# Optimization experiments

Measured on AMD Instinct MI355X. Metric: run time of the kernel, lower is better.

## Reference

```python
import jax, jax.numpy as jnp
import numpy as np


def setup_inputs() -> dict:
    key = jax.random.key(0)
    ks = jax.random.split(key, 8)
    B, T, D, H = 4, 4096, 1024, 64
    scale = D ** -0.5
    return {
        "x": jax.random.normal(ks[0], (B, T, D), dtype=jnp.float32),
        "mask": jax.random.randint(ks[1], (B, T), 0, 2, dtype=jnp.int32),
        "wq": jax.random.normal(ks[2], (H, D), dtype=jnp.float32) * scale,
        "bq": jax.random.normal(ks[3], (H,), dtype=jnp.float32) * 0.02,
        "wk": jax.random.normal(ks[4], (H, D), dtype=jnp.float32) * scale,
        "bk": jax.random.normal(ks[5], (H,), dtype=jnp.float32) * 0.02,
        "wv": jax.random.normal(ks[6], (H, D), dtype=jnp.float32) * scale,
        "bv": jax.random.normal(ks[7], (H,), dtype=jnp.float32) * 0.02,
    }


def reference(x, mask, wq, bq, wk, bk, wv, bv):
    # x: [B,T,D]; wq/wk/wv: [H,D] (torch Linear convention), mask: [B,T] int
    head_size = wq.shape[0]
    q = jnp.einsum("btd,hd->bth", x, wq) + bq  # [B,T,H]
    k = jnp.einsum("btd,hd->bth", x, wk) + bk
    v = jnp.einsum("btd,hd->bth", x, wv) + bv
    attn = jnp.einsum("bth,bsh->bts", q, k) * (head_size ** -0.5)  # [B,T,T]
    pad_mask = mask.astype(bool)[:, None, :]  # [B,1,T], True = keep
    attn = jnp.where(pad_mask, attn, jnp.float32(-1e9))
    attn = jax.nn.softmax(attn, axis=-1)
    # dropout is identity in eval/deterministic mode
    return jnp.einsum("bts,bsh->bth", attn, v)  # [B,T,H]
```

## Files before the change

kernel.cpp:

```cpp
#include <hip/hip_runtime.h>
#include <math.h>

#define BATCH 4
#define SEQ   4096
#define DIM   1024
#define HEAD  64
#define MROWS (BATCH*SEQ)
#define KT    64
#define QBLK  64

typedef __attribute__((ext_vector_type(8))) short short8;
typedef __attribute__((ext_vector_type(4))) float f32x4;

static __device__ __forceinline__ unsigned short f2b(float f) {
    union { float f; unsigned u; } v; v.f = f;
    return (unsigned short)((v.u + 0x7FFFu + ((v.u >> 16) & 1u)) >> 16);
}
static __device__ __forceinline__ unsigned cvtpk(float a, float b) {
    unsigned r;
    asm("v_cvt_pk_bf16_f32 %0, %1, %2" : "=v"(r) : "v"(a), "v"(b));
    return r;
}

#define QSC (0.125f * 1.4426950408889634f)
__global__ __launch_bounds__(256) void wconv_kernel(
    const float* __restrict__ wq, const float* __restrict__ bq,
    const float* __restrict__ wk, const float* __restrict__ bk,
    const float* __restrict__ wv, const float* __restrict__ bv,
    unsigned short* __restrict__ Wb, float* __restrict__ biasAll)
{
    int idx = blockIdx.x * 256 + threadIdx.x;
    int e   = idx * 4;
    int row = e >> 10;
    int col = e & 1023;
    const float* src = (row < 64) ? wq : (row < 128) ? wk : wv;
    float s = (row < 64) ? QSC : 1.0f;
    float4 g = *(const float4*)&src[(size_t)(row & 63) * DIM + col];
    ushort4 o;
    o.x = f2b(g.x * s); o.y = f2b(g.y * s); o.z = f2b(g.z * s); o.w = f2b(g.w * s);
    *(ushort4*)&Wb[e] = o;
    if (idx < 192) {
        const float* bs = (idx < 64) ? bq : (idx < 128) ? bk : bv;
        biasAll[idx] = bs[idx & 63] * ((idx < 64) ? QSC : 1.0f);
    }
}

#define NIT (DIM / 32)
__global__ __launch_bounds__(256) void qkvmm_kernel(
    const float* __restrict__ x, const unsigned short* __restrict__ Wb,
    const float* __restrict__ biasAll,
    unsigned short* __restrict__ qout, unsigned short* __restrict__ kout,
    unsigned short* __restrict__ vtout)
{
    __shared__ unsigned short xs[2][32 * 32];
    __shared__ unsigned short ws[2][192 * 32];

    const int tid  = threadIdx.x;
    const int m0   = blockIdx.x * 32;
    const int bb   = m0 >> 12;
    const int lane = tid & 63;
    const int w    = tid >> 6;
    const int lr   = lane & 15;
    const int lg   = lane >> 4;
    const int mrow  = (w >> 1) * 16;
    const int nbase = (w & 1) * 6;

    const int sxrow = tid >> 2, sxlg = tid & 3;
    int wn[3], wlg[3];
    #pragma unroll
    for (int i = 0; i < 3; ++i) { int idx = tid + i * 256; wn[i] = idx >> 2; wlg[i] = idx & 3; }

    f32x4 acc[6];
    #pragma unroll
    for (int nt = 0; nt < 6; ++nt) acc[nt] = (f32x4){0.f, 0.f, 0.f, 0.f};

    float4 xg0, xg1;
    short8 wg[3];

    auto LOADR = [&](int ko) {
        if (tid < 128) {
            const float* xp = &x[(size_t)(m0 + sxrow) * DIM + ko + sxlg * 8];
            xg0 = *(const float4*)xp;
            xg1 = *(const float4*)(xp + 4);
        }
        #pragma unroll
        for (int i = 0; i < 3; ++i)
            wg[i] = *(const short8*)&Wb[(size_t)wn[i] * DIM + ko + wlg[i] * 8];
    };
    auto WRITE = [&](int buf) {
        if (tid < 128) {
            uint4 c;
            c.x = cvtpk(xg0.x, xg0.y); c.y = cvtpk(xg0.z, xg0.w);
            c.z = cvtpk(xg1.x, xg1.y); c.w = cvtpk(xg1.z, xg1.w);
            *(uint4*)&xs[buf][sxrow * 32 + ((sxlg * 8) ^ ((sxrow & 3) * 8))] = c;
        }
        #pragma unroll
        for (int i = 0; i < 3; ++i)
            *(short8*)&ws[buf][wn[i] * 32 + ((wlg[i] * 8) ^ ((wn[i] & 3) * 8))] = wg[i];
    };

    LOADR(0);
    WRITE(0);
    __syncthreads();

    for (int it = 0; it < NIT; ++it) {
        if (it + 1 < NIT) LOADR((it + 1) * 32);
        const int cur = it & 1;
        const int arow = mrow + lr;
        short8 af = *(const short8*)&xs[cur][arow * 32 + ((lg * 8) ^ ((arow & 3) * 8))];
        #pragma unroll
        for (int nt = 0; nt < 6; ++nt) {
            int n = (nbase + nt) * 16 + lr;
            short8 bf = *(const short8*)&ws[cur][n * 32 + ((lg * 8) ^ ((n & 3) * 8))];
            acc[nt] = __builtin_amdgcn_mfma_f32_16x16x32_bf16(af, bf, acc[nt], 0, 0, 0);
        }
        if (it + 1 < NIT) WRITE((it + 1) & 1);
        __syncthreads();
    }

    #pragma unroll
    for (int nt = 0; nt < 6; ++nt) {
        int gn = (nbase + nt) * 16 + lr;
        float bv_ = biasAll[gn];
        #pragma unroll
        for (int r = 0; r < 4; ++r) {
            int grow = m0 + mrow + lg * 4 + r;
            unsigned short val = f2b(acc[nt][r] + bv_);
            if (gn < 64)       qout[(size_t)grow * HEAD + gn] = val;
            else if (gn < 128) kout[(size_t)grow * HEAD + gn - 64] = val;
            else {
                int t = (m0 & 4095) + mrow + lg * 4 + r;
                vtout[((size_t)bb * HEAD + gn - 128) * SEQ + t] = val;
            }
        }
    }
}

__global__ __launch_bounds__(256, 4) void flashmm_kernel(
    const unsigned short* __restrict__ qb, const unsigned short* __restrict__ kb,
    const unsigned short* __restrict__ vt, const int* __restrict__ mask,
    float* __restrict__ opart, float* __restrict__ mpart, float* __restrict__ lpart,
    int nsplit)
{
    const int b  = blockIdx.y;
    const int t0 = blockIdx.x * QBLK;
    const int z  = blockIdx.z;
    const int tid  = threadIdx.x;
    const int lane = tid & 63;
    const int w    = tid >> 6;
    const int lr = lane & 15;
    const int lg = lane >> 4;
    const int span = SEQ / nsplit;
    const int s_begin = z * span, s_end = s_begin + span;

    __shared__ unsigned short ks_l[KT * HEAD];
    __shared__ unsigned short vt_l[HEAD * KT];
    __shared__ unsigned short ps_l[4][16 * KT];
    __shared__ float mkf[KT];

    const unsigned short* qrow = qb + ((size_t)(b * SEQ + t0 + w * 16 + lr)) * HEAD;
    const short8 qf0 = *(const short8*)(qrow + lg * 8);
    const short8 qf1 = *(const short8*)(qrow + 32 + lg * 8);

    f32x4 acc_o[4];
    #pragma unroll
    for (int nt = 0; nt < 4; ++nt) acc_o[nt] = (f32x4){0.f, 0.f, 0.f, 0.f};
    float m_r = -INFINITY, l_r = 0.f;

    short8 kg[2], vg[2];
    float mgf = 0.f;

    auto LOADR = [&](int st) {
        #pragma unroll
        for (int i = 0; i < 2; ++i) {
            int c   = tid + i * 256;
            int row = c >> 3;
            int h0  = (c & 7) * 8;
            kg[i] = *(const short8*)(kb + ((size_t)(b * SEQ + st + row)) * HEAD + h0);
            vg[i] = *(const short8*)(vt + ((size_t)(b * HEAD + row)) * SEQ + st + h0);
        }
        if (tid < KT) mgf = (mask[(size_t)b * SEQ + st + tid] != 0) ? 0.f : -1e9f;
    };
    auto WRITE = [&]() {
        #pragma unroll
        for (int i = 0; i < 2; ++i) {
            int c   = tid + i * 256;
            int row = c >> 3;
            int h0  = (c & 7) * 8;
            *(short8*)&ks_l[row * HEAD + (h0 ^ ((row & 7) << 3))] = kg[i];
            *(short8*)&vt_l[row * KT + (h0 ^ ((row & 7) << 3))] = vg[i];
        }
        if (tid < KT) mkf[tid] = mgf;
    };

    LOADR(s_begin);
    for (int st = s_begin; st < s_end; st += KT) {
        __syncthreads();
        WRITE();
        __syncthreads();
        if (st + KT < s_end) LOADR(st + KT);

        f32x4 sT[4];
        __builtin_amdgcn_s_setprio(1);
        #pragma unroll
        for (int ct = 0; ct < 4; ++ct) {
            int krow = ct * 16 + lr;
            short8 kf0 = *(const short8*)&ks_l[krow * HEAD + ((lg * 8) ^ ((krow & 7) << 3))];
            short8 kf1 = *(const short8*)&ks_l[krow * HEAD + ((32 + lg * 8) ^ ((krow & 7) << 3))];
            f32x4 zz = (f32x4){0.f, 0.f, 0.f, 0.f};
            zz = __builtin_amdgcn_mfma_f32_16x16x32_bf16(kf0, qf0, zz, 0, 0, 0);
            zz = __builtin_amdgcn_mfma_f32_16x16x32_bf16(kf1, qf1, zz, 0, 0, 0);
            sT[ct] = zz;
        }
        __builtin_amdgcn_s_setprio(0);

        #pragma unroll
        for (int ct = 0; ct < 4; ++ct) {
            f32x4 mb = *(const f32x4*)&mkf[ct * 16 + lg * 4];
            sT[ct][0] += mb[0]; sT[ct][1] += mb[1];
            sT[ct][2] += mb[2]; sT[ct][3] += mb[3];
        }

        float mx = sT[0][0];
        #pragma unroll
        for (int ct = 0; ct < 4; ++ct)
            #pragma unroll
            for (int r = 0; r < 4; ++r) mx = fmaxf(mx, sT[ct][r]);
        mx = fmaxf(mx, __shfl_xor(mx, 16));
        mx = fmaxf(mx, __shfl_xor(mx, 32));

        bool defer = __all(mx <= m_r + 8.f);
        float base = defer ? m_r : fmaxf(m_r, mx);

        float rs = 0.f;
        #pragma unroll
        for (int ct = 0; ct < 4; ++ct)
            #pragma unroll
            for (int r = 0; r < 4; ++r) {
                float p = __builtin_amdgcn_exp2f(sT[ct][r] - base);
                sT[ct][r] = p;
                rs += p;
            }
        rs += __shfl_xor(rs, 16);
        rs += __shfl_xor(rs, 32);

        if (defer) {
            l_r += rs;
        } else {
            float sf = __builtin_amdgcn_exp2f(m_r - base);
            l_r = l_r * sf + rs;
            m_r = base;
            #pragma unroll
            for (int r = 0; r < 4; ++r) {
                float sfr = __shfl(sf, lg * 4 + r);
                #pragma unroll
                for (int nt = 0; nt < 4; ++nt) acc_o[nt][r] *= sfr;
            }
        }

        #pragma unroll
        for (int ct = 0; ct < 4; ++ct) {
            uint2 pk;
            pk.x = cvtpk(sT[ct][0], sT[ct][1]);
            pk.y = cvtpk(sT[ct][2], sT[ct][3]);
            *(uint2*)&ps_l[w][lr * KT + ((ct * 16 + lg * 4) ^ ((lr & 7) << 3))] = pk;
        }

        __builtin_amdgcn_s_setprio(1);
        #pragma unroll
        for (int kk = 0; kk < 2; ++kk) {
            int s0 = kk * 32 + lg * 8;
            short8 pf = *(const short8*)&ps_l[w][lr * KT + (s0 ^ ((lr & 7) << 3))];
            #pragma unroll
            for (int nt = 0; nt < 4; ++nt) {
                int hrow = nt * 16 + lr;
                short8 vf = *(const short8*)&vt_l[hrow * KT + (s0 ^ ((hrow & 7) << 3))];
                acc_o[nt] = __builtin_amdgcn_mfma_f32_16x16x32_bf16(pf, vf, acc_o[nt], 0, 0, 0);
            }
        }
        __builtin_amdgcn_s_setprio(0);
    }

    const size_t rbase = (size_t)z * MROWS + (size_t)b * SEQ + t0 + w * 16;
    const size_t obase = rbase * HEAD;
    #pragma unroll
    for (int nt = 0; nt < 4; ++nt)
        #pragma unroll
        for (int r = 0; r < 4; ++r) {
            int R = lg * 4 + r;
            opart[obase + (size_t)R * HEAD + nt * 16 + lr] = acc_o[nt][r];
        }
    if (lg == 0) {
        mpart[rbase + lr] = m_r;
        lpart[rbase + lr] = l_r;
    }
}

__global__ __launch_bounds__(256) void combine_kernel(
    const float* __restrict__ op, const float* __restrict__ mp,
    const float* __restrict__ lp, float* __restrict__ out, int nsplit)
{
    int idx = blockIdx.x * 256 + threadIdx.x;
    int row = idx >> 4;
    int h4  = (idx & 15) * 4;
    float mstar = -INFINITY;
    for (int s = 0; s < nsplit; ++s)
        mstar = fmaxf(mstar, mp[(size_t)s * MROWS + row]);
    float L = 0.f;
    float ax = 0.f, ay = 0.f, az = 0.f, aw = 0.f;
    for (int s = 0; s < nsplit; ++s) {
        float wgt = __builtin_amdgcn_exp2f(mp[(size_t)s * MROWS + row] - mstar);
        L += lp[(size_t)s * MROWS + row] * wgt;
        float4 o = *(const float4*)&op[((size_t)s * MROWS + row) * HEAD + h4];
        ax += o.x * wgt; ay += o.y * wgt; az += o.z * wgt; aw += o.w * wgt;
    }
    float r = 1.f / L;
    float4 res; res.x = ax * r; res.y = ay * r; res.z = az * r; res.w = aw * r;
    *(float4*)&out[(size_t)row * HEAD + h4] = res;
}

extern "C" void kernel_launch(void* const* d_in, const int* in_sizes, int n_in,
                              void* d_out, int out_size, void* d_ws, size_t ws_size,
                              hipStream_t stream) {
    const float* x    = (const float*)d_in[0];
    const int*   mask = (const int*)d_in[1];
    const float* wq   = (const float*)d_in[2];
    const float* bq   = (const float*)d_in[3];
    const float* wk   = (const float*)d_in[4];
    const float* bk   = (const float*)d_in[5];
    const float* wv   = (const float*)d_in[6];
    const float* bv   = (const float*)d_in[7];
    float* out = (float*)d_out;
    (void)in_sizes; (void)n_in; (void)out_size;

    const size_t NB = (size_t)MROWS * HEAD;
    unsigned short* qw  = (unsigned short*)d_ws;
    unsigned short* kw  = qw + NB;
    unsigned short* vtw = kw + NB;
    unsigned short* Wb  = vtw + NB;
    float* biasAll = (float*)(Wb + (size_t)192 * DIM);
    float* mpart   = biasAll + 192;

    const size_t base = 3 * NB * 2 + (size_t)192 * DIM * 2 + 192 * 4;
    const size_t per  = (size_t)MROWS * 8 + NB * 4;
    int KS = 1;
    if      (ws_size >= base + 8 * per) KS = 8;
    else if (ws_size >= base + 4 * per) KS = 4;
    else if (ws_size >= base + 2 * per) KS = 2;

    float* lpart = mpart + (size_t)KS * MROWS;
    float* opart = lpart + (size_t)KS * MROWS;

    wconv_kernel<<<dim3(192), 256, 0, stream>>>(wq, bq, wk, bk, wv, bv, Wb, biasAll);
    qkvmm_kernel<<<dim3(MROWS / 32), 256, 0, stream>>>(x, Wb, biasAll, qw, kw, vtw);
    flashmm_kernel<<<dim3(SEQ / QBLK, BATCH, KS), 256, 0, stream>>>(qw, kw, vtw, mask,
                                                                    opart, mpart, lpart, KS);
    combine_kernel<<<dim3(MROWS * 16 / 256), 256, 0, stream>>>(opart, mpart, lpart, out, KS);
}
```

Baseline: 80.41 us.

## Restructure QKV projection GEMM with direct global-to-LDS weight staging and register A

The QKV projection kernel now stages weight tiles with global_load_lds straight into a swizzled LDS buffer, using a 64-wide K step. Activations x are loaded directly into registers per wave and converted to bf16 there, instead of going through LDS. Blocks grow to 512 threads with 8 waves, each computing 3 N-tiles, and the K loop has half as many iterations and barriers. The aim is to cut LDS write traffic and VGPR staging for weights and to raise occupancy, at the cost of more redundant global loads of x across waves and a larger LDS footprint.

```diff
diff --git a/kernel.cpp b/kernel.cpp
--- a/kernel.cpp
+++ b/kernel.cpp
@@ -20,6 +20,11 @@
     unsigned r;
     asm("v_cvt_pk_bf16_f32 %0, %1, %2" : "=v"(r) : "v"(a), "v"(b));
     return r;
+}
+static __device__ __forceinline__ void gload_lds16(const void* g, void* l) {
+    __builtin_amdgcn_global_load_lds(
+        (const __attribute__((address_space(1))) unsigned int*)g,
+        (__attribute__((address_space(3))) unsigned int*)l, 16, 0, 0);
 }
 
 #define QSC (0.125f * 1.4426950408889634f)
@@ -45,15 +50,13 @@
     }
 }
 
-#define NIT (DIM / 32)
-__global__ __launch_bounds__(256) void qkvmm_kernel(
+__global__ __launch_bounds__(512, 4) void qkvmm_kernel(
     const float* __restrict__ x, const unsigned short* __restrict__ Wb,
     const float* __restrict__ biasAll,
     unsigned short* __restrict__ qout, unsigned short* __restrict__ kout,
     unsigned short* __restrict__ vtout)
 {
-    __shared__ unsigned short xs[2][32 * 32];
-    __shared__ unsigned short ws[2][192 * 32];
+    __shared__ unsigned short Wl[2][192 * 64];
 
     const int tid  = threadIdx.x;
     const int m0   = blockIdx.x * 32;
@@ -62,65 +65,69 @@
     const int w    = tid >> 6;
     const int lr   = lane & 15;
     const int lg   = lane >> 4;
-    const int mrow  = (w >> 1) * 16;
-    const int nbase = (w & 1) * 6;
-
-    const int sxrow = tid >> 2, sxlg = tid & 3;
-    int wn[3], wlg[3];
-    #pragma unroll
-    for (int i = 0; i < 3; ++i) { int idx = tid + i * 256; wn[i] = idx >> 2; wlg[i] = idx & 3; }
-
-    f32x4 acc[6];
-    #pragma unroll
-    for (int nt = 0; nt < 6; ++nt) acc[nt] = (f32x4){0.f, 0.f, 0.f, 0.f};
-
-    float4 xg0, xg1;
-    short8 wg[3];
-
-    auto LOADR = [&](int ko) {
-        if (tid < 128) {
-            const float* xp = &x[(size_t)(m0 + sxrow) * DIM + ko + sxlg * 8];
-            xg0 = *(const float4*)xp;
-            xg1 = *(const float4*)(xp + 4);
-        }
-        #pragma unroll
-        for (int i = 0; i < 3; ++i)
-            wg[i] = *(const short8*)&Wb[(size_t)wn[i] * DIM + ko + wlg[i] * 8];
+    const int mrow = (w >> 2) * 16;
+    const int nb0  = (w & 3) * 3;
+
+    int sn[3], scs[3];
+    #pragma unroll
+    for (int j = 0; j < 3; ++j) {
+        int L = j * 512 + tid;
+        sn[j] = L >> 3;
+        scs[j] = (L & 7) ^ (sn[j] & 7);
+    }
+    auto STAGE = [&](int buf, int ko) {
+        #pragma unroll
+        for (int j = 0; j < 3; ++j)
+            gload_lds16(Wb + (size_t)sn[j] * DIM + ko + scs[j] * 8,
+                        &Wl[buf][(size_t)(j * 512 + w * 64) * 8]);
     };
-    auto WRITE = [&](int buf) {
-        if (tid < 128) {
-            uint4 c;
-            c.x = cvtpk(xg0.x, xg0.y); c.y = cvtpk(xg0.z, xg0.w);
-            c.z = cvtpk(xg1.x, xg1.y); c.w = cvtpk(xg1.z, xg1.w);
-            *(uint4*)&xs[buf][sxrow * 32 + ((sxlg * 8) ^ ((sxrow & 3) * 8))] = c;
-        }
-        #pragma unroll
-        for (int i = 0; i < 3; ++i)
-            *(short8*)&ws[buf][wn[i] * 32 + ((wlg[i] * 8) ^ ((wn[i] & 3) * 8))] = wg[i];
+
+    const float* xrow = &x[(size_t)(m0 + mrow + lr) * DIM + lg * 8];
+    float4 aC0, aC1, aC2, aC3, aN0, aN1, aN2, aN3;
+    auto LOADA = [&](int ko, float4& d0, float4& d1, float4& d2, float4& d3) {
+        d0 = *(const float4*)(xrow + ko);
+        d1 = *(const float4*)(xrow + ko + 4);
+        d2 = *(const float4*)(xrow + ko + 32);
+        d3 = *(const float4*)(xrow + ko + 36);
     };
 
-    LOADR(0);
-    WRITE(0);
+    f32x4 acc[3];
+    #pragma unroll
+    for (int nt = 0; nt < 3; ++nt) acc[nt] = (f32x4){0.f, 0.f, 0.f, 0.f};
+
+    STAGE(0, 0);
+    LOADA(0, aC0, aC1, aC2, aC3);
     __syncthreads();
 
-    for (int it = 0; it < NIT; ++it) {
-        if (it + 1 < NIT) LOADR((it + 1) * 32);
+    for (int it = 0; it < 16; ++it) {
         const int cur = it & 1;
-        const int arow = mrow + lr;
-        short8 af = *(const short8*)&xs[cur][arow * 32 + ((lg * 8) ^ ((arow & 3) * 8))];
-        #pragma unroll
-        for (int nt = 0; nt < 6; ++nt) {
-            int n = (nbase + nt) * 16 + lr;
-            short8 bf = *(const short8*)&ws[cur][n * 32 + ((lg * 8) ^ ((n & 3) * 8))];
-            acc[nt] = __builtin_amdgcn_mfma_f32_16x16x32_bf16(af, bf, acc[nt], 0, 0, 0);
-        }
-        if (it + 1 < NIT) WRITE((it + 1) & 1);
+        if (it + 1 < 16) {
+            STAGE(cur ^ 1, (it + 1) * 64);
+            LOADA((it + 1) * 64, aN0, aN1, aN2, aN3);
+        }
+
+        union { unsigned u[4]; short8 s; } fa0, fa1;
+        fa0.u[0] = cvtpk(aC0.x, aC0.y); fa0.u[1] = cvtpk(aC0.z, aC0.w);
+        fa0.u[2] = cvtpk(aC1.x, aC1.y); fa0.u[3] = cvtpk(aC1.z, aC1.w);
+        fa1.u[0] = cvtpk(aC2.x, aC2.y); fa1.u[1] = cvtpk(aC2.z, aC2.w);
+        fa1.u[2] = cvtpk(aC3.x, aC3.y); fa1.u[3] = cvtpk(aC3.z, aC3.w);
+
+        #pragma unroll
+        for (int nt = 0; nt < 3; ++nt) {
+            int n = (nb0 + nt) * 16 + lr;
+            int base = n * 8;
+            short8 bf0 = *(const short8*)&Wl[cur][(size_t)(base + ((0 + lg) ^ (n & 7))) * 8];
+            short8 bf1 = *(const short8*)&Wl[cur][(size_t)(base + ((4 + lg) ^ (n & 7))) * 8];
+            acc[nt] = __builtin_amdgcn_mfma_f32_16x16x32_bf16(fa0.s, bf0, acc[nt], 0, 0, 0);
+            acc[nt] = __builtin_amdgcn_mfma_f32_16x16x32_bf16(fa1.s, bf1, acc[nt], 0, 0, 0);
+        }
         __syncthreads();
-    }
-
-    #pragma unroll
-    for (int nt = 0; nt < 6; ++nt) {
-        int gn = (nbase + nt) * 16 + lr;
+        aC0 = aN0; aC1 = aN1; aC2 = aN2; aC3 = aN3;
+    }
+
+    #pragma unroll
+    for (int nt = 0; nt < 3; ++nt) {
+        int gn = (nb0 + nt) * 16 + lr;
         float bv_ = biasAll[gn];
         #pragma unroll
         for (int r = 0; r < 4; ++r) {
@@ -352,7 +359,7 @@
     float* opart = lpart + (size_t)KS * MROWS;
 
     wconv_kernel<<<dim3(192), 256, 0, stream>>>(wq, bq, wk, bk, wv, bv, Wb, biasAll);
-    qkvmm_kernel<<<dim3(MROWS / 32), 256, 0, stream>>>(x, Wb, biasAll, qw, kw, vtw);
+    qkvmm_kernel<<<dim3(MROWS / 32), 512, 0, stream>>>(x, Wb, biasAll, qw, kw, vtw);
     flashmm_kernel<<<dim3(SEQ / QBLK, BATCH, KS), 256, 0, stream>>>(qw, kw, vtw, mask,
                                                                     opart, mpart, lpart, KS);
     combine_kernel<<<dim3(MROWS * 16 / 256), 256, 0, stream>>>(opart, mpart, lpart, out, KS);
```

After: 90.57 us. 1.13x slower.

## Load QKV projection operands directly into registers, dropping LDS staging

Applied to the files above, without the earlier changes.

The QKV projection kernel no longer stages x and weight tiles through double-buffered shared memory with barriers. Each lane now loads its MFMA fragments straight from global memory into registers, prefetching the next K-slice while the current one is computed. This removes LDS writes, LDS reads and __syncthreads, but each x row and weight row is now fetched by two waves instead of once per block, which raises global/L2 traffic and register pressure.

```diff
diff --git a/kernel.cpp b/kernel.cpp
--- a/kernel.cpp
+++ b/kernel.cpp
@@ -45,16 +45,12 @@
     }
 }
 
-#define NIT (DIM / 32)
 __global__ __launch_bounds__(256) void qkvmm_kernel(
     const float* __restrict__ x, const unsigned short* __restrict__ Wb,
     const float* __restrict__ biasAll,
     unsigned short* __restrict__ qout, unsigned short* __restrict__ kout,
     unsigned short* __restrict__ vtout)
 {
-    __shared__ unsigned short xs[2][32 * 32];
-    __shared__ unsigned short ws[2][192 * 32];
-
     const int tid  = threadIdx.x;
     const int m0   = blockIdx.x * 32;
     const int bb   = m0 >> 12;
@@ -62,65 +58,50 @@
     const int w    = tid >> 6;
     const int lr   = lane & 15;
     const int lg   = lane >> 4;
-    const int mrow  = (w >> 1) * 16;
-    const int nbase = (w & 1) * 6;
-
-    const int sxrow = tid >> 2, sxlg = tid & 3;
-    int wn[3], wlg[3];
-    #pragma unroll
-    for (int i = 0; i < 3; ++i) { int idx = tid + i * 256; wn[i] = idx >> 2; wlg[i] = idx & 3; }
+    const int mrow = (w >> 1) * 16;
+    const int nb0  = (w & 1) * 6;
+
+    const float* xrow = &x[(size_t)(m0 + mrow + lr) * DIM + lg * 8];
+    const unsigned short* wp[6];
+    #pragma unroll
+    for (int nt = 0; nt < 6; ++nt)
+        wp[nt] = Wb + (size_t)((nb0 + nt) * 16 + lr) * DIM + lg * 8;
 
     f32x4 acc[6];
     #pragma unroll
     for (int nt = 0; nt < 6; ++nt) acc[nt] = (f32x4){0.f, 0.f, 0.f, 0.f};
 
-    float4 xg0, xg1;
-    short8 wg[3];
-
-    auto LOADR = [&](int ko) {
-        if (tid < 128) {
-            const float* xp = &x[(size_t)(m0 + sxrow) * DIM + ko + sxlg * 8];
-            xg0 = *(const float4*)xp;
-            xg1 = *(const float4*)(xp + 4);
-        }
-        #pragma unroll
-        for (int i = 0; i < 3; ++i)
-            wg[i] = *(const short8*)&Wb[(size_t)wn[i] * DIM + ko + wlg[i] * 8];
-    };
-    auto WRITE = [&](int buf) {
-        if (tid < 128) {
-            uint4 c;
-            c.x = cvtpk(xg0.x, xg0.y); c.y = cvtpk(xg0.z, xg0.w);
-            c.z = cvtpk(xg1.x, xg1.y); c.w = cvtpk(xg1.z, xg1.w);
-            *(uint4*)&xs[buf][sxrow * 32 + ((sxlg * 8) ^ ((sxrow & 3) * 8))] = c;
-        }
-        #pragma unroll
-        for (int i = 0; i < 3; ++i)
-            *(short8*)&ws[buf][wn[i] * 32 + ((wlg[i] * 8) ^ ((wn[i] & 3) * 8))] = wg[i];
-    };
-
-    LOADR(0);
-    WRITE(0);
-    __syncthreads();
-
-    for (int it = 0; it < NIT; ++it) {
-        if (it + 1 < NIT) LOADR((it + 1) * 32);
-        const int cur = it & 1;
-        const int arow = mrow + lr;
-        short8 af = *(const short8*)&xs[cur][arow * 32 + ((lg * 8) ^ ((arow & 3) * 8))];
-        #pragma unroll
-        for (int nt = 0; nt < 6; ++nt) {
-            int n = (nbase + nt) * 16 + lr;
-            short8 bf = *(const short8*)&ws[cur][n * 32 + ((lg * 8) ^ ((n & 3) * 8))];
-            acc[nt] = __builtin_amdgcn_mfma_f32_16x16x32_bf16(af, bf, acc[nt], 0, 0, 0);
-        }
-        if (it + 1 < NIT) WRITE((it + 1) & 1);
-        __syncthreads();
+    float4 xc0, xc1, xn0, xn1;
+    short8 wc[6], wn[6];
+
+    xc0 = *(const float4*)(xrow);
+    xc1 = *(const float4*)(xrow + 4);
+    #pragma unroll
+    for (int nt = 0; nt < 6; ++nt) wc[nt] = *(const short8*)(wp[nt]);
+
+    #pragma unroll 2
+    for (int it = 0; it < 32; ++it) {
+        const int kn = (it + 1) * 32;
+        if (it + 1 < 32) {
+            xn0 = *(const float4*)(xrow + kn);
+            xn1 = *(const float4*)(xrow + kn + 4);
+            #pragma unroll
+            for (int nt = 0; nt < 6; ++nt) wn[nt] = *(const short8*)(wp[nt] + kn);
+        }
+        union { unsigned u[4]; short8 s; } fa;
+        fa.u[0] = cvtpk(xc0.x, xc0.y); fa.u[1] = cvtpk(xc0.z, xc0.w);
+        fa.u[2] = cvtpk(xc1.x, xc1.y); fa.u[3] = cvtpk(xc1.z, xc1.w);
+        #pragma unroll
+        for (int nt = 0; nt < 6; ++nt)
+            acc[nt] = __builtin_amdgcn_mfma_f32_16x16x32_bf16(fa.s, wc[nt], acc[nt], 0, 0, 0);
+        xc0 = xn0; xc1 = xn1;
+        #pragma unroll
+        for (int nt = 0; nt < 6; ++nt) wc[nt] = wn[nt];
     }
 
     #pragma unroll
     for (int nt = 0; nt < 6; ++nt) {
-        int gn = (nbase + nt) * 16 + lr;
+        int gn = (nb0 + nt) * 16 + lr;
         float bv_ = biasAll[gn];
         #pragma unroll
         for (int r = 0; r < 4; ++r) {
```

Result: slower. 112.7 us (+40.2%).

## Deepen QKV projection global-load pipeline to three stages and cap split-K at four

Applied to the files above, without the earlier changes.

The QKV projection GEMM now prefetches global tiles three iterations ahead into register ring buffers and writes the next LDS buffer before the current MFMAs. It replaces __syncthreads with a custom waitcnt plus barrier and fully unrolls the K loop, so global latency is hidden behind more in-flight loads. Separately, the flash attention key split is capped at 4 instead of 8, which shrinks partial-result traffic and combine work but reduces grid parallelism. The extra register ring buffers and the full unroll raise register pressure. Writing the next buffer before compute relies on the end-of-iteration barrier to keep the two LDS buffers consistent.

```diff
diff --git a/kernel.cpp b/kernel.cpp
--- a/kernel.cpp
+++ b/kernel.cpp
@@ -20,6 +20,10 @@
     unsigned r;
     asm("v_cvt_pk_bf16_f32 %0, %1, %2" : "=v"(r) : "v"(a), "v"(b));
     return r;
+}
+static __device__ __forceinline__ void lds_barrier() {
+    asm volatile("s_waitcnt lgkmcnt(0)" ::: "memory");
+    __builtin_amdgcn_s_barrier();
 }
 
 #define QSC (0.125f * 1.4426950408889634f)
@@ -74,38 +78,41 @@
     #pragma unroll
     for (int nt = 0; nt < 6; ++nt) acc[nt] = (f32x4){0.f, 0.f, 0.f, 0.f};
 
-    float4 xg0, xg1;
-    short8 wg[3];
-
-    auto LOADR = [&](int ko) {
+    float4 xg0[3], xg1[3];
+    short8 wg0[3], wg1[3], wg2[3];
+
+    auto LOADR = [&](int ko, int s) {
         if (tid < 128) {
             const float* xp = &x[(size_t)(m0 + sxrow) * DIM + ko + sxlg * 8];
-            xg0 = *(const float4*)xp;
-            xg1 = *(const float4*)(xp + 4);
-        }
-        #pragma unroll
-        for (int i = 0; i < 3; ++i)
-            wg[i] = *(const short8*)&Wb[(size_t)wn[i] * DIM + ko + wlg[i] * 8];
+            xg0[s] = *(const float4*)xp;
+            xg1[s] = *(const float4*)(xp + 4);
+        }
+        wg0[s] = *(const short8*)&Wb[(size_t)wn[0] * DIM + ko + wlg[0] * 8];
+        wg1[s] = *(const short8*)&Wb[(size_t)wn[1] * DIM + ko + wlg[1] * 8];
+        wg2[s] = *(const short8*)&Wb[(size_t)wn[2] * DIM + ko + wlg[2] * 8];
     };
-    auto WRITE = [&](int buf) {
+    auto WRITE = [&](int buf, int s) {
         if (tid < 128) {
             uint4 c;
-            c.x = cvtpk(xg0.x, xg0.y); c.y = cvtpk(xg0.z, xg0.w);
-            c.z = cvtpk(xg1.x, xg1.y); c.w = cvtpk(xg1.z, xg1.w);
+            c.x = cvtpk(xg0[s].x, xg0[s].y); c.y = cvtpk(xg0[s].z, xg0[s].w);
+            c.z = cvtpk(xg1[s].x, xg1[s].y); c.w = cvtpk(xg1[s].z, xg1[s].w);
             *(uint4*)&xs[buf][sxrow * 32 + ((sxlg * 8) ^ ((sxrow & 3) * 8))] = c;
         }
-        #pragma unroll
-        for (int i = 0; i < 3; ++i)
-            *(short8*)&ws[buf][wn[i] * 32 + ((wlg[i] * 8) ^ ((wn[i] & 3) * 8))] = wg[i];
+        *(short8*)&ws[buf][wn[0] * 32 + ((wlg[0] * 8) ^ ((wn[0] & 3) * 8))] = wg0[s];
+        *(short8*)&ws[buf][wn[1] * 32 + ((wlg[1] * 8) ^ ((wn[1] & 3) * 8))] = wg1[s];
+        *(short8*)&ws[buf][wn[2] * 32 + ((wlg[2] * 8) ^ ((wn[2] & 3) * 8))] = wg2[s];
     };
 
-    LOADR(0);
-    WRITE(0);
-    __syncthreads();
-
+    LOADR(0, 0); LOADR(32, 1); LOADR(64, 2);
+    WRITE(0, 0);
+    lds_barrier();
+
+    #pragma unroll
     for (int it = 0; it < NIT; ++it) {
-        if (it + 1 < NIT) LOADR((it + 1) * 32);
         const int cur = it & 1;
+        if (it + 3 < NIT) LOADR((it + 3) * 32, (it + 3) % 3);
+        if (it + 1 < NIT) WRITE(cur ^ 1, (it + 1) % 3);
+
         const int arow = mrow + lr;
         short8 af = *(const short8*)&xs[cur][arow * 32 + ((lg * 8) ^ ((arow & 3) * 8))];
         #pragma unroll
@@ -114,8 +121,7 @@
             short8 bf = *(const short8*)&ws[cur][n * 32 + ((lg * 8) ^ ((n & 3) * 8))];
             acc[nt] = __builtin_amdgcn_mfma_f32_16x16x32_bf16(af, bf, acc[nt], 0, 0, 0);
         }
-        if (it + 1 < NIT) WRITE((it + 1) & 1);
-        __syncthreads();
+        lds_barrier();
     }
 
     #pragma unroll
@@ -344,8 +350,7 @@
     const size_t base = 3 * NB * 2 + (size_t)192 * DIM * 2 + 192 * 4;
     const size_t per  = (size_t)MROWS * 8 + NB * 4;
     int KS = 1;
-    if      (ws_size >= base + 8 * per) KS = 8;
-    else if (ws_size >= base + 4 * per) KS = 4;
+    if      (ws_size >= base + 4 * per) KS = 4;
     else if (ws_size >= base + 2 * per) KS = 2;
 
     float* lpart = mpart + (size_t)KS * MROWS;
```

New measurement: 71.48 us (median of 2 runs). -11.1%, faster.
